# Kernel tuning notes

Measured on AMD Instinct MI355X. Metric: run time of the kernel, lower is better.

## Reference

```python
import jax, jax.numpy as jnp
import numpy as np

B, P, G, C = 64, 5000, 300, 20   # images, preds/img, gt/img, num classes
INPUT_SIZE = 512.0
IOU_THRESH = 0.5


def setup_inputs() -> dict:
    key = jax.random.key(0)
    k1, k2, k3, k4, k5, k6, k7 = jax.random.split(key, 7)
    # predictions: [x1,y1,x2,y2,score,cls], boxes normalized to [0,1]
    pxy = jax.random.uniform(k1, (B, P, 2), minval=0.0, maxval=0.8)
    pwh = jax.random.uniform(k2, (B, P, 2), minval=0.02, maxval=0.2)
    score = jax.random.uniform(k3, (B, P, 1))
    pcls = jax.random.randint(k4, (B, P, 1), 0, C).astype(jnp.float32)
    output = jnp.concatenate([pxy, pxy + pwh, score, pcls], axis=-1)
    # ground truth: [x1,y1,x2,y2,cls]
    txy = jax.random.uniform(k5, (B, G, 2), minval=0.0, maxval=0.8)
    twh = jax.random.uniform(k6, (B, G, 2), minval=0.02, maxval=0.2)
    tcls = jax.random.randint(k7, (B, G, 1), 0, C).astype(jnp.float32)
    labels = jnp.concatenate([txy, txy + twh, tcls], axis=-1)
    return {"output": output, "labels": labels}


def reference(output, labels):
    scale = jnp.array([INPUT_SIZE, INPUT_SIZE, INPUT_SIZE, INPUT_SIZE], dtype=output.dtype)

    def match_image(preds, targets):  # preds [P,6], targets [G,5]
        tcls = targets[:, 4]
        tboxes = targets[:, :4] * scale                     # [G,4]
        tarea = (tboxes[:, 2] - tboxes[:, 0]) * (tboxes[:, 3] - tboxes[:, 1])

        def step(detected, pred):
            pbox = pred[:4] * scale
            lt = jnp.maximum(pbox[:2], tboxes[:, :2])       # [G,2]
            rb = jnp.minimum(pbox[2:], tboxes[:, 2:])
            wh = jnp.clip(rb - lt, 0.0)
            inter = wh[:, 0] * wh[:, 1]
            parea = (pbox[2] - pbox[0]) * (pbox[3] - pbox[1])
            ious = inter / (parea + tarea - inter)          # [G]
            cls_mask = tcls == pred[5]
            masked = jnp.where(cls_mask, ious, -1.0)
            bi = jnp.argmax(masked)                          # greedy argmax over same-class gt
            match = ((pred[4] > 0)
                     & jnp.any(cls_mask)
                     & (masked[bi] > IOU_THRESH)
                     & (~detected[bi]))                      # sequential dedup
            detected = detected.at[bi].set(detected[bi] | match)
            return detected, match

        _, correct = jax.lax.scan(step, jnp.zeros(tboxes.shape[0], dtype=bool), preds)
        return correct                                       # [P] bool

    correct = jax.vmap(match_image)(output, labels).astype(output.dtype)  # [B,P]
    # stats: (correct flag, score, predicted class) per prediction; tcls per image
    stats = jnp.stack([correct, output[:, :, 4], output[:, :, 5]], axis=-1)  # [B,P,3]
    tcls = labels[:, :, 4]                                                    # [B,G]
    return stats, tcls
```

## Files before the change

kernel.cpp:

```cpp
#include <hip/hip_runtime.h>
#include <cstdint>

#define B 64
#define P 5000
#define G 300
#define C 20
#define SCALE_F 512.0f
#define IOU_TH 0.5f
#define NSPLIT 16
#define PCHUNK ((P + NSPLIT - 1) / NSPLIT)
#define NTA 256
#define SPT ((PCHUNK + NTA - 1) / NTA)
#define SENT 0x7FFFFFFF

#pragma clang fp contract(off)

__global__ __launch_bounds__(NTA, 4) void match_kernel(
    const float* __restrict__ preds,
    const float* __restrict__ labels,
    int* __restrict__ blockfp,
    float* __restrict__ out_stats,
    float* __restrict__ out_tcls)
{
    const int s = blockIdx.x;
    const int b = blockIdx.y;
    const int tid = threadIdx.x;

    __shared__ float4 sb[G];
    __shared__ float  sa[G];
    __shared__ short  ssi[G];
    __shared__ short  cls_s[G];
    __shared__ int    so[C + 1];
    __shared__ int    cnt[C];
    __shared__ int    pcnt[C];
    __shared__ int    firstp[G];
    __shared__ unsigned short psorted[PCHUNK];

    const float* lab = labels + (size_t)b * G * 5;
    const float* prd = preds + (size_t)b * P * 6;
    const int pbase = s * PCHUNK;
    const int pend = (pbase + PCHUNK < P) ? pbase + PCHUNK : P;
    const int npred = pend - pbase;

    if (tid < C) { cnt[tid] = 0; pcnt[tid] = 0; }
    for (int t = tid; t < G; t += NTA) {
        float cf = lab[t * 5 + 4];
        cls_s[t] = (short)(int)cf;
        firstp[t] = SENT;
        if (s == 0) out_tcls[(size_t)b * G + t] = cf;
    }
    __syncthreads();

    for (int t = tid; t < G; t += NTA) atomicAdd(&cnt[cls_s[t]], 1);
    int myc[SPT];
    #pragma unroll
    for (int k = 0; k < SPT; ++k) {
        myc[k] = -1;
        int p = pbase + k * NTA + tid;
        if (p < pend) {
            float2 sc = *reinterpret_cast<const float2*>(prd + (size_t)p * 6 + 4);
            int c = (int)sc.y;
            myc[k] = c;
            atomicAdd(&pcnt[c], 1);
            size_t ip3 = ((size_t)b * P + p) * 3;
            out_stats[ip3 + 0] = 0.0f;
            out_stats[ip3 + 1] = sc.x;
            out_stats[ip3 + 2] = sc.y;
        }
    }
    __syncthreads();

    if (tid == 0) {
        int a = 0;
        for (int c = 0; c < C; ++c) { so[c] = a; a += cnt[c]; }
        so[C] = a;
    }
    if (tid == 64) {
        int a = 0;
        for (int c = 0; c < C; ++c) { int v = pcnt[c]; pcnt[c] = a; a += v; }
    }
    __syncthreads();

    for (int t = tid; t < G; t += NTA) {
        short c = cls_s[t];
        int rank = 0;
        for (int u = 0; u < t; ++u) rank += (cls_s[u] == c) ? 1 : 0;
        int pos = so[c] + rank;
        float x1 = lab[t * 5 + 0] * SCALE_F;
        float y1 = lab[t * 5 + 1] * SCALE_F;
        float x2 = lab[t * 5 + 2] * SCALE_F;
        float y2 = lab[t * 5 + 3] * SCALE_F;
        sb[pos] = make_float4(x1, y1, x2, y2);
        sa[pos] = (x2 - x1) * (y2 - y1);
        ssi[pos] = (short)t;
    }
    #pragma unroll
    for (int k = 0; k < SPT; ++k) {
        int p = pbase + k * NTA + tid;
        if (p < pend) {
            int pos = atomicAdd(&pcnt[myc[k]], 1);
            psorted[pos] = (unsigned short)p;
        }
    }
    __syncthreads();

    #pragma unroll
    for (int k = 0; k < SPT; ++k) {
        int slot = k * NTA + tid;
        if (slot >= npred) continue;
        int p = psorted[slot];
        const float* pr = prd + (size_t)p * 6;
        float2 q0 = *reinterpret_cast<const float2*>(pr);
        float2 q1 = *reinterpret_cast<const float2*>(pr + 2);
        float2 q2 = *reinterpret_cast<const float2*>(pr + 4);
        float px1 = q0.x * SCALE_F;
        float py1 = q0.y * SCALE_F;
        float px2 = q1.x * SCALE_F;
        float py2 = q1.y * SCALE_F;
        float score = q2.x;
        int c = (int)q2.y;
        float parea = (px2 - px1) * (py2 - py1);

        int lo = so[c], hi = so[c + 1];
        float best = -1.0f;
        int bi = -1;
        for (int j = lo; j < hi; ++j) {
            float4 tb = sb[j];
            float lx = fmaxf(px1, tb.x);
            float ly = fmaxf(py1, tb.y);
            float rx = fminf(px2, tb.z);
            float ry = fminf(py2, tb.w);
            float w = fmaxf(rx - lx, 0.0f);
            float h = fmaxf(ry - ly, 0.0f);
            float inter = w * h;
            float uni = (parea + sa[j]) - inter;
            float iou = inter / uni;
            if (iou > best) { best = iou; bi = ssi[j]; }
        }

        bool eligible = (score > 0.0f) && (hi > lo) && (best > IOU_TH);
        if (eligible) atomicMin(&firstp[bi], p);
    }
    __syncthreads();

    for (int t = tid; t < G; t += NTA)
        blockfp[((size_t)b * NSPLIT + s) * G + t] = firstp[t];
}

__global__ __launch_bounds__(512) void resolve_kernel(
    const int* __restrict__ blockfp,
    float* __restrict__ out_stats)
{
    const int b = blockIdx.x;
    const int t = threadIdx.x;
    if (t >= G) return;

    const int* fp = blockfp + (size_t)b * NSPLIT * G + t;
    int m = fp[0];
    #pragma unroll
    for (int s = 1; s < NSPLIT; ++s) m = min(m, fp[s * G]);

    if (m != SENT)
        out_stats[((size_t)b * P + m) * 3] = 1.0f;
}

extern "C" void kernel_launch(void* const* d_in, const int* in_sizes, int n_in,
                              void* d_out, int out_size, void* d_ws, size_t ws_size,
                              hipStream_t stream) {
    const float* output = (const float*)d_in[0];
    const float* labels = (const float*)d_in[1];

    float* out_stats = (float*)d_out;
    float* out_tcls  = (float*)d_out + (size_t)B * P * 3;

    int* blockfp = (int*)d_ws;

    dim3 grid(NSPLIT, B);
    match_kernel<<<grid, NTA, 0, stream>>>(output, labels, blockfp,
                                           out_stats, out_tcls);
    resolve_kernel<<<dim3(B), 512, 0, stream>>>(blockfp, out_stats);
}
```

Before: 82.31 us.

## Replace quadratic GT rank scan with ballot-based ranking and retune split/block sizes

Replaces the O(G^2) per-thread rank loop for sorting ground-truth boxes by class with a per-64-chunk class histogram plus wavefront ballot and popcount ranking. It also halves the prediction splits to 8 and doubles the block size to 512, so each GT element is handled by one thread. This removes the serial rank cost in setup, but it adds one barrier and gives fewer, larger blocks (512 total), which may lower occupancy and latency hiding in the matching phase.

New measurement: 70.31 us. 1.17x faster.

```diff
diff --git a/kernel.cpp b/kernel.cpp
--- a/kernel.cpp
+++ b/kernel.cpp
@@ -7,10 +7,11 @@
 #define C 20
 #define SCALE_F 512.0f
 #define IOU_TH 0.5f
-#define NSPLIT 16
+#define NSPLIT 8
 #define PCHUNK ((P + NSPLIT - 1) / NSPLIT)
-#define NTA 256
+#define NTA 512
 #define SPT ((PCHUNK + NTA - 1) / NTA)
+#define NCHUNK ((G + 63) / 64)
 #define SENT 0x7FFFFFFF
 
 #pragma clang fp contract(off)
@@ -30,8 +31,9 @@
     __shared__ float  sa[G];
     __shared__ short  ssi[G];
     __shared__ short  cls_s[G];
+    __shared__ int    chist[NCHUNK][C];
+    __shared__ int    cnt[C];
     __shared__ int    so[C + 1];
-    __shared__ int    cnt[C];
     __shared__ int    pcnt[C];
     __shared__ int    firstp[G];
     __shared__ unsigned short psorted[PCHUNK];
@@ -42,16 +44,17 @@
     const int pend = (pbase + PCHUNK < P) ? pbase + PCHUNK : P;
     const int npred = pend - pbase;
 
-    if (tid < C) { cnt[tid] = 0; pcnt[tid] = 0; }
-    for (int t = tid; t < G; t += NTA) {
-        float cf = lab[t * 5 + 4];
-        cls_s[t] = (short)(int)cf;
-        firstp[t] = SENT;
-        if (s == 0) out_tcls[(size_t)b * G + t] = cf;
-    }
-    __syncthreads();
-
-    for (int t = tid; t < G; t += NTA) atomicAdd(&cnt[cls_s[t]], 1);
+    if (tid < NCHUNK * C) ((int*)chist)[tid] = 0;
+    if (tid < C) pcnt[tid] = 0;
+    if (tid < G) {
+        float cf = lab[tid * 5 + 4];
+        cls_s[tid] = (short)(int)cf;
+        firstp[tid] = SENT;
+        if (s == 0) out_tcls[(size_t)b * G + tid] = cf;
+    }
+    __syncthreads();
+
+    if (tid < G) atomicAdd(&chist[tid >> 6][cls_s[tid]], 1);
     int myc[SPT];
     #pragma unroll
     for (int k = 0; k < SPT; ++k) {
@@ -70,29 +73,48 @@
     }
     __syncthreads();
 
+    if (tid < C) {
+        int run = 0;
+        #pragma unroll
+        for (int w = 0; w < NCHUNK; ++w) {
+            int v = chist[w][tid]; chist[w][tid] = run; run += v;
+        }
+        cnt[tid] = run;
+    }
+    if (tid == 64) {
+        int a = 0;
+        for (int c = 0; c < C; ++c) { int v = pcnt[c]; pcnt[c] = a; a += v; }
+    }
+    __syncthreads();
+
     if (tid == 0) {
         int a = 0;
         for (int c = 0; c < C; ++c) { so[c] = a; a += cnt[c]; }
         so[C] = a;
     }
-    if (tid == 64) {
-        int a = 0;
-        for (int c = 0; c < C; ++c) { int v = pcnt[c]; pcnt[c] = a; a += v; }
-    }
-    __syncthreads();
-
-    for (int t = tid; t < G; t += NTA) {
-        short c = cls_s[t];
-        int rank = 0;
-        for (int u = 0; u < t; ++u) rank += (cls_s[u] == c) ? 1 : 0;
-        int pos = so[c] + rank;
-        float x1 = lab[t * 5 + 0] * SCALE_F;
-        float y1 = lab[t * 5 + 1] * SCALE_F;
-        float x2 = lab[t * 5 + 2] * SCALE_F;
-        float y2 = lab[t * 5 + 3] * SCALE_F;
-        sb[pos] = make_float4(x1, y1, x2, y2);
-        sa[pos] = (x2 - x1) * (y2 - y1);
-        ssi[pos] = (short)t;
+    __syncthreads();
+
+    if (tid < NCHUNK * 64) {
+        int c = (tid < G) ? (int)cls_s[tid] : -1;
+        unsigned long long mymask = 0;
+        #pragma unroll
+        for (int cc = 0; cc < C; ++cc) {
+            unsigned long long m = __ballot(c == cc);
+            if (c == cc) mymask = m;
+        }
+        if (tid < G) {
+            int lane = tid & 63;
+            int rank = chist[tid >> 6][c]
+                     + __popcll(mymask & ((1ull << lane) - 1));
+            int pos = so[c] + rank;
+            float x1 = lab[tid * 5 + 0] * SCALE_F;
+            float y1 = lab[tid * 5 + 1] * SCALE_F;
+            float x2 = lab[tid * 5 + 2] * SCALE_F;
+            float y2 = lab[tid * 5 + 3] * SCALE_F;
+            sb[pos] = make_float4(x1, y1, x2, y2);
+            sa[pos] = (x2 - x1) * (y2 - y1);
+            ssi[pos] = (short)tid;
+        }
     }
     #pragma unroll
     for (int k = 0; k < SPT; ++k) {
@@ -143,8 +165,8 @@
     }
     __syncthreads();
 
-    for (int t = tid; t < G; t += NTA)
-        blockfp[((size_t)b * NSPLIT + s) * G + t] = firstp[t];
+    if (tid < G)
+        blockfp[((size_t)b * NSPLIT + s) * G + tid] = firstp[tid];
 }
 
 __global__ __launch_bounds__(512) void resolve_kernel(
```
